# Kernel optimization log

Measured on AMD Instinct MI355X. Metric: run time of the kernel, lower is better.

## Reference

```python
import jax, jax.numpy as jnp
import numpy as np
from jax import lax

B, N, C = 8, 4096, 64
RATIO = 0.25
M = int(N * RATIO)          # sampled centers per cloud (fps ratio)
K = 64                      # max_num_neighbors in ball query
R = 0.2                     # ball_query_radius
H = 128                     # MLP width
NEG = jnp.float32(-1e30)


def setup_inputs() -> dict:
    key = jax.random.key(0)
    k1, k2, k3, k4 = jax.random.split(key, 4)
    x = jax.random.normal(k1, (B, N, C), jnp.float32)
    pos = jax.random.uniform(k2, (B, N, 3), jnp.float32)  # unit cube coords
    W1 = jax.random.normal(k3, (C + 3, H), jnp.float32) * 0.05
    b1 = jnp.zeros((H,), jnp.float32)
    W2 = jax.random.normal(k4, (H, H), jnp.float32) * 0.05
    b2 = jnp.zeros((H,), jnp.float32)
    return {"x": x, "pos": pos, "W1": W1, "b1": b1, "W2": W2, "b2": b2}


def _fps(pos):
    """Farthest point sampling on one cloud [N,3] -> M int32 indices (start at 0)."""
    d0 = jnp.sum((pos - pos[0]) ** 2, axis=-1)  # min sq-dist to selected set
    def step(mind, _):
        nxt = jnp.argmax(mind).astype(jnp.int32)
        d = jnp.sum((pos - pos[nxt]) ** 2, axis=-1)
        return jnp.minimum(mind, d), nxt
    _, idxs = lax.scan(step, d0, None, length=M - 1)
    return jnp.concatenate([jnp.zeros((1,), jnp.int32), idxs])


def reference(x, pos, W1, b1, W2, b2):
    # --- FPS sampling (per cloud, deterministic start) ---
    idx = jax.vmap(_fps)(pos)                      # [B,M]
    bidx = jnp.arange(B)[:, None]
    centers = pos[bidx, idx]                        # [B,M,3]

    # --- ball query: first K points within radius R of each center ---
    d2 = jnp.sum((centers[:, :, None, :] - pos[:, None, :, :]) ** 2, axis=-1)  # [B,M,N]
    in_ball = d2 <= R * R
    # prefer lowest index (torch_cluster radius returns up to K arbitrary/first hits)
    score = jnp.where(in_ball, -jnp.arange(N, dtype=jnp.float32), NEG)
    vals, nbr = lax.top_k(score, K)                 # nbr: [B,M,K] neighbor indices
    valid = vals > NEG / 2                          # [B,M,K]; center itself always valid

    # --- PointNetConv: gather -> local MLP on [x_j, pos_j - pos_i] -> max aggr ---
    b3 = jnp.arange(B)[:, None, None]
    xj = x[b3, nbr]                                  # [B,M,K,C]
    rel = pos[b3, nbr] - centers[:, :, None, :]      # [B,M,K,3]
    feat = jnp.concatenate([xj, rel], axis=-1)       # [B,M,K,C+3]
    h = jax.nn.relu(feat @ W1 + b1)
    h = jax.nn.relu(h @ W2 + b2)                     # [B,M,K,H]
    h = jnp.where(valid[..., None], h, NEG)
    out = jnp.max(h, axis=2)                          # [B,M,H] max aggregation
    return out, centers
```

## Files before the change

### kernel.cpp

```cpp
#include <hip/hip_runtime.h>

#define BN 8
#define NN 4096
#define CC 64
#define MM 1024
#define KK 64
#define HH 128

typedef __attribute__((ext_vector_type(8))) short short8;
typedef __attribute__((ext_vector_type(4))) float f32x4;
typedef __attribute__((ext_vector_type(2))) float f32x2;
typedef unsigned long long u64;
typedef unsigned int u32;

__device__ inline unsigned short f2bf(float f) {
  union { float f; unsigned u; } v; v.f = f;
  unsigned r = v.u + 0x7FFFu + ((v.u >> 16) & 1u);
  return (unsigned short)(r >> 16);
}

__device__ inline float sqd(float ax, float ay, float az, float bx, float by, float bz) {
  float dx = __fsub_rn(ax, bx), dy = __fsub_rn(ay, by), dz = __fsub_rn(az, bz);
  return __fadd_rn(__fadd_rn(__fmul_rn(dx, dx), __fmul_rn(dy, dy)), __fmul_rn(dz, dz));
}

__global__ void prep_w(const float* __restrict__ W1, const float* __restrict__ W2,
                       short* __restrict__ W1T, short* __restrict__ W2T) {
  int t = blockIdx.x * 256 + threadIdx.x;
  if (t < 128 * 104) {
    int n = t / 104, k = t % 104;
    float v = (k < 67) ? W1[k * 128 + n] : 0.f;
    W1T[t] = (short)f2bf(v);
  }
  if (t < 128 * 136) {
    int n = t / 136, k = t % 136;
    float v = (k < 128) ? W2[k * 128 + n] : 0.f;
    W2T[t] = (short)f2bf(v);
  }
}

template <int CTRL, int RM>
__device__ __forceinline__ float dppf(float x) {
  int v = __builtin_amdgcn_update_dpp(0, __float_as_int(x), CTRL, RM, 0xF, false);
  return __int_as_float(v);
}

__device__ __forceinline__ float wave_fmax(float x) {
  x = fmaxf(x, dppf<0xB1, 0xF>(x));
  x = fmaxf(x, dppf<0x4E, 0xF>(x));
  x = fmaxf(x, dppf<0x141, 0xF>(x));
  x = fmaxf(x, dppf<0x140, 0xF>(x));
  x = fmaxf(x, dppf<0x142, 0xA>(x));
  x = fmaxf(x, dppf<0x143, 0xC>(x));
  return __int_as_float(__builtin_amdgcn_readlane(__float_as_int(x), 63));
}

__global__ __launch_bounds__(512) void fps_k(const float* __restrict__ pos,
                                             float* __restrict__ centers) {
  const int b = blockIdx.x;
  const int tid = threadIdx.x;
  const int lane = tid & 63;
  const int wv = tid >> 6;
  __shared__ f32x4 sp4[NN];
  __shared__ f32x4 svm4[2];
  __shared__ u32 sminp[2];

  const float* P = pos + (size_t)b * NN * 3;

  f32x2 X[4], Y[4], Z[4], M[4];
#pragma unroll
  for (int j = 0; j < 4; ++j) {
    int p0 = tid * 8 + j * 2;
    float x0 = P[p0 * 3 + 0], y0 = P[p0 * 3 + 1], z0 = P[p0 * 3 + 2];
    float x1 = P[p0 * 3 + 3], y1 = P[p0 * 3 + 4], z1 = P[p0 * 3 + 5];
    X[j].x = x0; X[j].y = x1;
    Y[j].x = y0; Y[j].y = y1;
    Z[j].x = z0; Z[j].y = z1;
    f32x4 v0; v0[0] = x0; v0[1] = y0; v0[2] = z0; v0[3] = 0.f;
    f32x4 v1; v1[0] = x1; v1[1] = y1; v1[2] = z1; v1[3] = 0.f;
    sp4[p0] = v0;
    sp4[p0 + 1] = v1;
  }
#pragma unroll
  for (int j = 0; j < 4; ++j)
    asm volatile("" : "+v"(X[j]), "+v"(Y[j]), "+v"(Z[j]));

  const float c0x = P[0], c0y = P[1], c0z = P[2];
  {
#pragma clang fp contract(off)
    f32x2 cx; cx.x = c0x; cx.y = c0x;
    f32x2 cy; cy.x = c0y; cy.y = c0y;
    f32x2 cz; cz.x = c0z; cz.y = c0z;
#pragma unroll
    for (int j = 0; j < 4; ++j) {
      f32x2 dx = X[j] - cx, dy = Y[j] - cy, dz = Z[j] - cz;
      M[j] = (dx * dx + dy * dy) + dz * dz;
    }
  }

  if (tid == 0) {
    centers[(size_t)(b * MM) * 3 + 0] = c0x;
    centers[(size_t)(b * MM) * 3 + 1] = c0y;
    centers[(size_t)(b * MM) * 3 + 2] = c0z;
    sminp[0] = 0xFFFFFFFFu;
    sminp[1] = 0xFFFFFFFFu;
  }
  __syncthreads();

  for (int m = 1; m < MM; ++m) {
    float mv = fmaxf(fmaxf(fmaxf(M[0].x, M[0].y), fmaxf(M[1].x, M[1].y)),
                     fmaxf(fmaxf(M[2].x, M[2].y), fmaxf(M[3].x, M[3].y)));
    float wmax = wave_fmax(mv);
    if (lane == 0) ((float*)svm4)[wv] = wmax;
    __syncthreads();
    f32x4 s0 = svm4[0], s1 = svm4[1];
    float bmax = fmaxf(fmaxf(fmaxf(s0[0], s0[1]), fmaxf(s0[2], s0[3])),
                       fmaxf(fmaxf(s1[0], s1[1]), fmaxf(s1[2], s1[3])));
    if (mv == bmax) {
      u32 em = 0;
#pragma unroll
      for (int j = 0; j < 4; ++j) {
        if (M[j].x == bmax) em |= 1u << (2 * j);
        if (M[j].y == bmax) em |= 1u << (2 * j + 1);
      }
      atomicMin(&sminp[m & 1], (u32)(tid * 8 + (int)__builtin_ctz(em)));
    }
    if (tid == 0) sminp[(m + 1) & 1] = 0xFFFFFFFFu;
    __syncthreads();
    const u32 bp = sminp[m & 1];
    const f32x4 c4 = sp4[bp];
    if (tid == 0) {
      centers[(size_t)(b * MM + m) * 3 + 0] = c4[0];
      centers[(size_t)(b * MM + m) * 3 + 1] = c4[1];
      centers[(size_t)(b * MM + m) * 3 + 2] = c4[2];
    }
    {
#pragma clang fp contract(off)
      f32x2 cx; cx.x = c4[0]; cx.y = c4[0];
      f32x2 cy; cy.x = c4[1]; cy.y = c4[1];
      f32x2 cz; cz.x = c4[2]; cz.y = c4[2];
#pragma unroll
      for (int j = 0; j < 4; ++j) {
        f32x2 dx = X[j] - cx, dy = Y[j] - cy, dz = Z[j] - cz;
        f32x2 d2 = (dx * dx + dy * dy) + dz * dz;
        M[j].x = fminf(M[j].x, d2.x);
        M[j].y = fminf(M[j].y, d2.y);
      }
    }
  }
}

__global__ __launch_bounds__(256) void sa_k(const float* __restrict__ x,
                                            const float* __restrict__ pos,
                                            const float* __restrict__ b1,
                                            const float* __restrict__ b2,
                                            const short* __restrict__ W1T,
                                            const short* __restrict__ W2T,
                                            const float* __restrict__ centers,
                                            float* __restrict__ out) {
  const int cm = blockIdx.x;
  const int b = cm >> 10;
  const int tid = threadIdx.x;
  const int lane = tid & 63, wv = tid >> 6;
  const int l15 = lane & 15, lg = lane >> 4;

  __shared__ short s_feat[64][104];
  __shared__ short s_h1[64][136];
  __shared__ int s_nbr[64];
  __shared__ int s_wcnt[4];

  const int n0 = wv * 32;
  short8 w1f[2][3], w2f[2][4];
#pragma unroll
  for (int nt = 0; nt < 2; ++nt) {
    int row = n0 + nt * 16 + l15;
#pragma unroll
    for (int kt = 0; kt < 3; ++kt)
      w1f[nt][kt] = *reinterpret_cast<const short8*>(W1T + row * 104 + kt * 32 + lg * 8);
#pragma unroll
    for (int kt = 0; kt < 4; ++kt)
      w2f[nt][kt] = *reinterpret_cast<const short8*>(W2T + row * 136 + kt * 32 + lg * 8);
  }

  const float* Pb = pos + (size_t)b * NN * 3;
  const float cx = centers[(size_t)cm * 3 + 0];
  const float cy = centers[(size_t)cm * 3 + 1];
  const float cz = centers[(size_t)cm * 3 + 2];

  int cnt = 0;
  for (int base = 0; base < NN; base += 256) {
    int p = base + tid;
    float d2 = sqd(Pb[p * 3 + 0], Pb[p * 3 + 1], Pb[p * 3 + 2], cx, cy, cz);
    bool pred = d2 <= 0.04f;
    unsigned long long mask = __ballot(pred);
    if (lane == 0) s_wcnt[wv] = __popcll(mask);
    __syncthreads();
    int wbase = cnt, tot = 0;
#pragma unroll
    for (int w = 0; w < 4; ++w) {
      int c = s_wcnt[w];
      tot += c;
      if (w < wv) wbase += c;
    }
    if (pred) {
      int slot = wbase + (int)__popcll(mask & ((1ull << lane) - 1ull));
      if (slot < KK) s_nbr[slot] = p;
    }
    cnt += tot;
    __syncthreads();
    if (cnt >= KK) break;
  }
  if (cnt > KK) cnt = KK;

  {
    int* fz = (int*)&s_feat[0][0];
    for (int i = tid; i < 64 * 104 / 2; i += 256) fz[i] = 0;
  }
  __syncthreads();

  {
    const int j = tid >> 2, q = tid & 3;
    if (j < cnt) {
      int nj = s_nbr[j];
      const float* xr = x + ((size_t)b * NN + nj) * CC + q * 16;
      unsigned* dst = (unsigned*)&s_feat[j][q * 16];
#pragma unroll
      for (int v4 = 0; v4 < 4; ++v4) {
        f32x4 xv = *reinterpret_cast<const f32x4*>(xr + v4 * 4);
        unsigned lo0 = (unsigned)f2bf(xv[0]) | ((unsigned)f2bf(xv[1]) << 16);
        unsigned lo1 = (unsigned)f2bf(xv[2]) | ((unsigned)f2bf(xv[3]) << 16);
        dst[v4 * 2 + 0] = lo0;
        dst[v4 * 2 + 1] = lo1;
      }
      if (q == 0) {
        s_feat[j][64] = (short)f2bf(__fsub_rn(Pb[nj * 3 + 0], cx));
        s_feat[j][65] = (short)f2bf(__fsub_rn(Pb[nj * 3 + 1], cy));
        s_feat[j][66] = (short)f2bf(__fsub_rn(Pb[nj * 3 + 2], cz));
      }
    }
  }
  __syncthreads();

  f32x4 acc[4][2];
#pragma unroll
  for (int mt = 0; mt < 4; ++mt)
#pragma unroll
    for (int nt = 0; nt < 2; ++nt) acc[mt][nt] = (f32x4)0.f;

#pragma unroll
  for (int mt = 0; mt < 4; ++mt) {
    int arow = mt * 16 + l15;
#pragma unroll
    for (int kt = 0; kt < 3; ++kt) {
      short8 af = *reinterpret_cast<const short8*>(&s_feat[arow][kt * 32 + lg * 8]);
      acc[mt][0] = __builtin_amdgcn_mfma_f32_16x16x32_bf16(af, w1f[0][kt], acc[mt][0], 0, 0, 0);
      acc[mt][1] = __builtin_amdgcn_mfma_f32_16x16x32_bf16(af, w1f[1][kt], acc[mt][1], 0, 0, 0);
    }
  }

#pragma unroll
  for (int mt = 0; mt < 4; ++mt) {
#pragma unroll
    for (int nt = 0; nt < 2; ++nt) {
      int col = n0 + nt * 16 + l15;
      float bias = b1[col];
#pragma unroll
      for (int r = 0; r < 4; ++r) {
        int row = mt * 16 + lg * 4 + r;
        float h = fmaxf(__fadd_rn(acc[mt][nt][r], bias), 0.f);
        s_h1[row][col] = (short)f2bf(h);
      }
    }
  }
  __syncthreads();

  f32x4 acc2[4][2];
#pragma unroll
  for (int mt = 0; mt < 4; ++mt)
#pragma unroll
    for (int nt = 0; nt < 2; ++nt) acc2[mt][nt] = (f32x4)0.f;

#pragma unroll
  for (int mt = 0; mt < 4; ++mt) {
    int arow = mt * 16 + l15;
#pragma unroll
    for (int kt = 0; kt < 4; ++kt) {
      short8 af = *reinterpret_cast<const short8*>(&s_h1[arow][kt * 32 + lg * 8]);
      acc2[mt][0] = __builtin_amdgcn_mfma_f32_16x16x32_bf16(af, w2f[0][kt], acc2[mt][0], 0, 0, 0);
      acc2[mt][1] = __builtin_amdgcn_mfma_f32_16x16x32_bf16(af, w2f[1][kt], acc2[mt][1], 0, 0, 0);
    }
  }

#pragma unroll
  for (int nt = 0; nt < 2; ++nt) {
    int col = n0 + nt * 16 + l15;
    float bias = b2[col];
    float mx = -1e30f;
#pragma unroll
    for (int mt = 0; mt < 4; ++mt) {
#pragma unroll
      for (int r = 0; r < 4; ++r) {
        int row = mt * 16 + lg * 4 + r;
        float h = fmaxf(__fadd_rn(acc2[mt][nt][r], bias), 0.f);
        if (row < cnt) mx = fmaxf(mx, h);
      }
    }
    mx = fmaxf(mx, __shfl_xor(mx, 16));
    mx = fmaxf(mx, __shfl_xor(mx, 32));
    if (lg == 0) out[(size_t)cm * HH + col] = mx;
  }
}

extern "C" void kernel_launch(void* const* d_in, const int* in_sizes, int n_in,
                              void* d_out, int out_size, void* d_ws, size_t ws_size,
                              hipStream_t stream) {
  const float* x = (const float*)d_in[0];
  const float* pos = (const float*)d_in[1];
  const float* W1 = (const float*)d_in[2];
  const float* b1 = (const float*)d_in[3];
  const float* W2 = (const float*)d_in[4];
  const float* b2 = (const float*)d_in[5];

  float* out = (float*)d_out;
  float* centers = out + (size_t)BN * MM * HH;

  char* ws = (char*)d_ws;
  short* W1T = (short*)ws;
  short* W2T = (short*)(ws + 26624);

  prep_w<<<68, 256, 0, stream>>>(W1, W2, W1T, W2T);
  fps_k<<<BN, 512, 0, stream>>>(pos, centers);
  sa_k<<<BN * MM, 256, 0, stream>>>(x, pos, b1, b2, W1T, W2T, centers, out);
}
```

Baseline: 834.1 us.

## Run farthest point sampling in a single wavefront without block barriers

The FPS kernel now runs one 64-lane wave per cloud instead of 512 threads. Each lane holds 64 points in registers, and the argmax uses a wave reduction plus ballot and readlane. This removes the two __syncthreads and the shared-memory atomicMin from each of the 1023 serial iterations. Centers are buffered in LDS and written out once at the end. The trade is that each wave now does eight times more per-iteration arithmetic on one SIMD, with much higher register pressure.

```diff
diff --git a/kernel.cpp b/kernel.cpp
--- a/kernel.cpp
+++ b/kernel.cpp
@@ -55,99 +55,128 @@
   return __int_as_float(__builtin_amdgcn_readlane(__float_as_int(x), 63));
 }
 
-__global__ __launch_bounds__(512) void fps_k(const float* __restrict__ pos,
+__global__ __launch_bounds__(64) void fps1_k(const float* __restrict__ pos,
                                              float* __restrict__ centers) {
   const int b = blockIdx.x;
-  const int tid = threadIdx.x;
-  const int lane = tid & 63;
-  const int wv = tid >> 6;
-  __shared__ f32x4 sp4[NN];
-  __shared__ f32x4 svm4[2];
-  __shared__ u32 sminp[2];
+  const int lane = threadIdx.x;
+  __shared__ __align__(16) f32x4 sp4[NN];
+  __shared__ float scen[MM * 3];
 
   const float* P = pos + (size_t)b * NN * 3;
 
-  f32x2 X[4], Y[4], Z[4], M[4];
-#pragma unroll
-  for (int j = 0; j < 4; ++j) {
-    int p0 = tid * 8 + j * 2;
-    float x0 = P[p0 * 3 + 0], y0 = P[p0 * 3 + 1], z0 = P[p0 * 3 + 2];
-    float x1 = P[p0 * 3 + 3], y1 = P[p0 * 3 + 4], z1 = P[p0 * 3 + 5];
-    X[j].x = x0; X[j].y = x1;
-    Y[j].x = y0; Y[j].y = y1;
-    Z[j].x = z0; Z[j].y = z1;
-    f32x4 v0; v0[0] = x0; v0[1] = y0; v0[2] = z0; v0[3] = 0.f;
-    f32x4 v1; v1[0] = x1; v1[1] = y1; v1[2] = z1; v1[3] = 0.f;
-    sp4[p0] = v0;
-    sp4[p0 + 1] = v1;
-  }
-#pragma unroll
-  for (int j = 0; j < 4; ++j)
-    asm volatile("" : "+v"(X[j]), "+v"(Y[j]), "+v"(Z[j]));
+  f32x2 X[32], Y[32], Z[32], M[32];
+
+  const float* Px = P + (size_t)lane * 96;
+  const float* Py = P + (size_t)2048 * 3 + (size_t)lane * 96;
+#pragma unroll
+  for (int g = 0; g < 8; ++g) {
+    f32x4 v0 = *(const f32x4*)(Px + 12 * g + 0);
+    f32x4 v1 = *(const f32x4*)(Px + 12 * g + 4);
+    f32x4 v2 = *(const f32x4*)(Px + 12 * g + 8);
+    X[4 * g + 0].x = v0[0]; Y[4 * g + 0].x = v0[1]; Z[4 * g + 0].x = v0[2];
+    X[4 * g + 1].x = v0[3]; Y[4 * g + 1].x = v1[0]; Z[4 * g + 1].x = v1[1];
+    X[4 * g + 2].x = v1[2]; Y[4 * g + 2].x = v1[3]; Z[4 * g + 2].x = v2[0];
+    X[4 * g + 3].x = v2[1]; Y[4 * g + 3].x = v2[2]; Z[4 * g + 3].x = v2[3];
+    int p0 = lane * 32 + 4 * g;
+    f32x4 w;
+    w[0] = v0[0]; w[1] = v0[1]; w[2] = v0[2]; w[3] = 0.f; sp4[p0 + 0] = w;
+    w[0] = v0[3]; w[1] = v1[0]; w[2] = v1[1]; w[3] = 0.f; sp4[p0 + 1] = w;
+    w[0] = v1[2]; w[1] = v1[3]; w[2] = v2[0]; w[3] = 0.f; sp4[p0 + 2] = w;
+    w[0] = v2[1]; w[1] = v2[2]; w[2] = v2[3]; w[3] = 0.f; sp4[p0 + 3] = w;
+  }
+#pragma unroll
+  for (int g = 0; g < 8; ++g) {
+    f32x4 v0 = *(const f32x4*)(Py + 12 * g + 0);
+    f32x4 v1 = *(const f32x4*)(Py + 12 * g + 4);
+    f32x4 v2 = *(const f32x4*)(Py + 12 * g + 8);
+    X[4 * g + 0].y = v0[0]; Y[4 * g + 0].y = v0[1]; Z[4 * g + 0].y = v0[2];
+    X[4 * g + 1].y = v0[3]; Y[4 * g + 1].y = v1[0]; Z[4 * g + 1].y = v1[1];
+    X[4 * g + 2].y = v1[2]; Y[4 * g + 2].y = v1[3]; Z[4 * g + 2].y = v2[0];
+    X[4 * g + 3].y = v2[1]; Y[4 * g + 3].y = v2[2]; Z[4 * g + 3].y = v2[3];
+    int p0 = 2048 + lane * 32 + 4 * g;
+    f32x4 w;
+    w[0] = v0[0]; w[1] = v0[1]; w[2] = v0[2]; w[3] = 0.f; sp4[p0 + 0] = w;
+    w[0] = v0[3]; w[1] = v1[0]; w[2] = v1[1]; w[3] = 0.f; sp4[p0 + 1] = w;
+    w[0] = v1[2]; w[1] = v1[3]; w[2] = v2[0]; w[3] = 0.f; sp4[p0 + 2] = w;
+    w[0] = v2[1]; w[1] = v2[2]; w[2] = v2[3]; w[3] = 0.f; sp4[p0 + 3] = w;
+  }
+  __syncthreads();
 
   const float c0x = P[0], c0y = P[1], c0z = P[2];
+  if (lane == 0) { scen[0] = c0x; scen[1] = c0y; scen[2] = c0z; }
+  f32x2 E;
+  float mv;
   {
 #pragma clang fp contract(off)
-    f32x2 cx; cx.x = c0x; cx.y = c0x;
-    f32x2 cy; cy.x = c0y; cy.y = c0y;
-    f32x2 cz; cz.x = c0z; cz.y = c0z;
-#pragma unroll
-    for (int j = 0; j < 4; ++j) {
-      f32x2 dx = X[j] - cx, dy = Y[j] - cy, dz = Z[j] - cz;
+    f32x2 vcx; vcx.x = c0x; vcx.y = c0x;
+    f32x2 vcy; vcy.x = c0y; vcy.y = c0y;
+    f32x2 vcz; vcz.x = c0z; vcz.y = c0z;
+#pragma unroll
+    for (int j = 0; j < 32; ++j) {
+      f32x2 dx = X[j] - vcx, dy = Y[j] - vcy, dz = Z[j] - vcz;
       M[j] = (dx * dx + dy * dy) + dz * dz;
     }
-  }
-
-  if (tid == 0) {
-    centers[(size_t)(b * MM) * 3 + 0] = c0x;
-    centers[(size_t)(b * MM) * 3 + 1] = c0y;
-    centers[(size_t)(b * MM) * 3 + 2] = c0z;
-    sminp[0] = 0xFFFFFFFFu;
-    sminp[1] = 0xFFFFFFFFu;
-  }
-  __syncthreads();
+    f32x2 A[16];
+#pragma unroll
+    for (int i = 0; i < 16; ++i) A[i] = __builtin_elementwise_max(M[2 * i], M[2 * i + 1]);
+#pragma unroll
+    for (int i = 0; i < 8; ++i) A[i] = __builtin_elementwise_max(A[2 * i], A[2 * i + 1]);
+#pragma unroll
+    for (int i = 0; i < 4; ++i) A[i] = __builtin_elementwise_max(A[2 * i], A[2 * i + 1]);
+    A[0] = __builtin_elementwise_max(A[0], A[1]);
+    E = __builtin_elementwise_max(A[0], __builtin_elementwise_max(A[2], A[3]));
+    mv = fmaxf(E.x, E.y);
+  }
 
   for (int m = 1; m < MM; ++m) {
-    float mv = fmaxf(fmaxf(fmaxf(M[0].x, M[0].y), fmaxf(M[1].x, M[1].y)),
-                     fmaxf(fmaxf(M[2].x, M[2].y), fmaxf(M[3].x, M[3].y)));
     float wmax = wave_fmax(mv);
-    if (lane == 0) ((float*)svm4)[wv] = wmax;
-    __syncthreads();
-    f32x4 s0 = svm4[0], s1 = svm4[1];
-    float bmax = fmaxf(fmaxf(fmaxf(s0[0], s0[1]), fmaxf(s0[2], s0[3])),
-                       fmaxf(fmaxf(s1[0], s1[1]), fmaxf(s1[2], s1[3])));
-    if (mv == bmax) {
-      u32 em = 0;
-#pragma unroll
-      for (int j = 0; j < 4; ++j) {
-        if (M[j].x == bmax) em |= 1u << (2 * j);
-        if (M[j].y == bmax) em |= 1u << (2 * j + 1);
-      }
-      atomicMin(&sminp[m & 1], (u32)(tid * 8 + (int)__builtin_ctz(em)));
-    }
-    if (tid == 0) sminp[(m + 1) & 1] = 0xFFFFFFFFu;
-    __syncthreads();
-    const u32 bp = sminp[m & 1];
-    const f32x4 c4 = sp4[bp];
-    if (tid == 0) {
-      centers[(size_t)(b * MM + m) * 3 + 0] = c4[0];
-      centers[(size_t)(b * MM + m) * 3 + 1] = c4[1];
-      centers[(size_t)(b * MM + m) * 3 + 2] = c4[2];
+    u64 bx = __ballot(E.x == wmax);
+    u64 by = __ballot(E.y == wmax);
+    const bool hb = (bx != 0);
+    u64 bal = hb ? bx : by;
+    int L = (int)__builtin_ctzll(bal);
+    u32 r = 63u;
+    if (hb) {
+#pragma unroll
+      for (int j = 31; j >= 0; --j) r = (M[j].x == wmax) ? (u32)j : r;
+    } else {
+#pragma unroll
+      for (int j = 31; j >= 0; --j) r = (M[j].y == wmax) ? (u32)j : r;
+    }
+    u32 rW = (u32)__builtin_amdgcn_readlane((int)r, L);
+    int bp = (hb ? 0 : 2048) + L * 32 + (int)rW;
+    f32x4 c4 = sp4[bp];
+    if (lane == 0) {
+      scen[m * 3 + 0] = c4[0];
+      scen[m * 3 + 1] = c4[1];
+      scen[m * 3 + 2] = c4[2];
     }
     {
 #pragma clang fp contract(off)
-      f32x2 cx; cx.x = c4[0]; cx.y = c4[0];
-      f32x2 cy; cy.x = c4[1]; cy.y = c4[1];
-      f32x2 cz; cz.x = c4[2]; cz.y = c4[2];
-#pragma unroll
-      for (int j = 0; j < 4; ++j) {
-        f32x2 dx = X[j] - cx, dy = Y[j] - cy, dz = Z[j] - cz;
+      f32x2 vcx; vcx.x = c4[0]; vcx.y = c4[0];
+      f32x2 vcy; vcy.x = c4[1]; vcy.y = c4[1];
+      f32x2 vcz; vcz.x = c4[2]; vcz.y = c4[2];
+#pragma unroll
+      for (int j = 0; j < 32; ++j) {
+        f32x2 dx = X[j] - vcx, dy = Y[j] - vcy, dz = Z[j] - vcz;
         f32x2 d2 = (dx * dx + dy * dy) + dz * dz;
-        M[j].x = fminf(M[j].x, d2.x);
-        M[j].y = fminf(M[j].y, d2.y);
-      }
-    }
-  }
+        M[j] = __builtin_elementwise_min(M[j], d2);
+      }
+      f32x2 A[16];
+#pragma unroll
+      for (int i = 0; i < 16; ++i) A[i] = __builtin_elementwise_max(M[2 * i], M[2 * i + 1]);
+#pragma unroll
+      for (int i = 0; i < 8; ++i) A[i] = __builtin_elementwise_max(A[2 * i], A[2 * i + 1]);
+#pragma unroll
+      for (int i = 0; i < 4; ++i) A[i] = __builtin_elementwise_max(A[2 * i], A[2 * i + 1]);
+      A[0] = __builtin_elementwise_max(A[0], A[1]);
+      E = __builtin_elementwise_max(A[0], __builtin_elementwise_max(A[2], A[3]));
+      mv = fmaxf(E.x, E.y);
+    }
+  }
+  __syncthreads();
+  for (int i = lane; i < MM * 3; i += 64)
+    centers[(size_t)b * MM * 3 + i] = scen[i];
 }
 
 __global__ __launch_bounds__(256) void sa_k(const float* __restrict__ x,
@@ -329,6 +358,6 @@
   short* W2T = (short*)(ws + 26624);
 
   prep_w<<<68, 256, 0, stream>>>(W1, W2, W1T, W2T);
-  fps_k<<<BN, 512, 0, stream>>>(pos, centers);
+  fps1_k<<<BN, 64, 0, stream>>>(pos, centers);
   sa_k<<<BN * MM, 256, 0, stream>>>(x, pos, b1, b2, W1T, W2T, centers, out);
 }
```

Result: slower. 1.364 ms (+63.6%).
